# Optimization experiments

Hardware: AMD Instinct MI355X
Metric: run time of the kernel (lower is better)

## Reference

```python
import jax, jax.numpy as jnp
import numpy as np

N, P, C, M = 64, 8732, 91, 20          # batch, n_priors (SSD300), n_classes, padded objects/image
THRESHOLD = 0.5
NEG_POS_RATIO = 3
ALPHA = 1.0


def setup_inputs() -> dict:
    key = jax.random.key(0)
    k = jax.random.split(key, 7)
    predicted_locs = jax.random.normal(k[0], (N, P, 4), jnp.float32)
    predicted_scores = jax.random.normal(k[1], (N, P, C), jnp.float32)
    # ground-truth boxes in boundary (x1,y1,x2,y2) format, valid fractional coords
    xy = jax.random.uniform(k[2], (N, M, 2), minval=0.0, maxval=0.6)
    wh = jax.random.uniform(k[3], (N, M, 2), minval=0.05, maxval=0.4)
    boxes = jnp.concatenate([xy, xy + wh], axis=-1)
    labels = jax.random.randint(k[4], (N, M), 1, C).astype(jnp.int32)  # 0 = background
    # prior boxes in center-size (cx,cy,w,h) format
    cxy = jax.random.uniform(k[5], (P, 2), minval=0.05, maxval=0.95)
    pwh = jax.random.uniform(k[6], (P, 2), minval=0.05, maxval=0.3)
    priors_cxcy = jnp.concatenate([cxy, pwh], axis=-1)
    return dict(predicted_locs=predicted_locs, predicted_scores=predicted_scores,
                boxes=boxes, labels=labels, priors_cxcy=priors_cxcy)


def _iou(a, b):
    # a: (M,4) xyxy, b: (P,4) xyxy -> (M,P)
    lo = jnp.maximum(a[:, None, :2], b[None, :, :2])
    hi = jnp.minimum(a[:, None, 2:], b[None, :, 2:])
    inter = jnp.clip(hi - lo, 0.0).prod(-1)
    area_a = (a[:, 2:] - a[:, :2]).prod(-1)
    area_b = (b[:, 2:] - b[:, :2]).prod(-1)
    return inter / (area_a[:, None] + area_b[None, :] - inter)


def _xy_to_cxcy(xy):
    return jnp.concatenate([(xy[..., :2] + xy[..., 2:]) * 0.5, xy[..., 2:] - xy[..., :2]], -1)


def _cxcy_to_gcxgcy(cxcy, priors):
    g_cxcy = (cxcy[..., :2] - priors[..., :2]) / (priors[..., 2:] / 10.0)
    g_wh = jnp.log(cxcy[..., 2:] / priors[..., 2:]) * 5.0
    return jnp.concatenate([g_cxcy, g_wh], -1)


def _match_one(boxes_i, labels_i, priors_cxcy, priors_xy):
    overlap = _iou(boxes_i, priors_xy)                    # (M, P)
    ov_per_prior = overlap.max(0)                         # (P,)
    obj_per_prior = overlap.argmax(0)                     # (P,)
    prior_per_obj = overlap.argmax(1)                     # (M,)
    # force each object onto its best prior with overlap 1
    obj_per_prior = obj_per_prior.at[prior_per_obj].set(jnp.arange(M))
    ov_per_prior = ov_per_prior.at[prior_per_obj].set(1.0)
    label_per_prior = labels_i[obj_per_prior]             # (P,)
    label_per_prior = jnp.where(ov_per_prior < THRESHOLD, 0, label_per_prior)
    true_locs = _cxcy_to_gcxgcy(_xy_to_cxcy(boxes_i[obj_per_prior]), priors_cxcy)  # (P,4)
    return label_per_prior, true_locs


def reference(predicted_locs, predicted_scores, boxes, labels, priors_cxcy):
    priors_xy = jnp.concatenate([priors_cxcy[:, :2] - priors_cxcy[:, 2:] * 0.5,
                                 priors_cxcy[:, :2] + priors_cxcy[:, 2:] * 0.5], -1)
    true_classes, true_locs = jax.vmap(_match_one, in_axes=(0, 0, None, None))(
        boxes, labels, priors_cxcy, priors_xy)            # (N,P), (N,P,4)

    pos = true_classes != 0                               # (N, P)
    n_pos = pos.sum(1)                                    # (N,)
    n_pos_total = n_pos.sum().astype(jnp.float32)

    # localization: smooth L1 (beta=1), mean over positive elements
    d = predicted_locs - true_locs
    sl1 = jnp.where(jnp.abs(d) < 1.0, 0.5 * d * d, jnp.abs(d) - 0.5)   # (N,P,4)
    loc_loss = (sl1 * pos[..., None]).sum() / (n_pos_total * 4.0)

    # confidence: per-prior cross entropy
    logp = jax.nn.log_softmax(predicted_scores, axis=-1)  # (N,P,C)
    ce = -jnp.take_along_axis(logp, true_classes[..., None], axis=-1)[..., 0]  # (N,P)

    conf_loss_pos = (ce * pos).sum()
    # hard negative mining: sort negative losses desc, take 3*n_pos per image
    ce_neg = jnp.where(pos, 0.0, ce)
    ce_neg_sorted = jnp.sort(ce_neg, axis=1)[:, ::-1]     # (N,P) descending
    hard_neg = jnp.arange(P)[None, :] < (NEG_POS_RATIO * n_pos)[:, None]
    conf_loss_hard_neg = (ce_neg_sorted * hard_neg).sum()

    conf_loss = (conf_loss_pos + conf_loss_hard_neg) / n_pos_total
    return conf_loss + ALPHA * loc_loss
```

## Files before the change

### kernel.cpp

```cpp
#include <hip/hip_runtime.h>

#define NN 64
#define PP 8732
#define CC 91
#define MM 20
#define RATIO 3
#define BPI 8
#define CHUNK 1092
#define ROWS 128
#define BTHR 512
#define TILES2 ((NN * PP) / ROWS)

typedef unsigned long long u64;

__global__ __launch_bounds__(256) void match_a(
    const float4* __restrict__ boxes4,
    const float4* __restrict__ priors4,
    float* __restrict__ iou_out,
    unsigned char* __restrict__ obj8,
    u64* __restrict__ combined_part)
{
  __shared__ float bx0[MM], by0[MM], bx1[MM], by1[MM], ba[MM];
  __shared__ u64 wkey[4][MM];
  const int blk = blockIdx.x, tid = threadIdx.x;
  const int wave = tid >> 6, lane = tid & 63;
  const int n = blk >> 3, part = blk & 7;
  const int c0 = part * CHUNK;
  const int cend = (c0 + CHUNK < PP) ? c0 + CHUNK : PP;

  if (tid < MM) {
    float4 b = boxes4[n * MM + tid];
    bx0[tid] = b.x; by0[tid] = b.y; bx1[tid] = b.z; by1[tid] = b.w;
    ba[tid] = (b.z - b.x) * (b.w - b.y);
  }
  __syncthreads();

  float bi[MM], bd[MM]; int bpp[MM];
#pragma unroll
  for (int m = 0; m < MM; ++m) { bi[m] = 0.0f; bd[m] = 1.0f; bpp[m] = 0; }

#pragma unroll
  for (int i = 0; i < 5; ++i) {
    int p = c0 + tid + i * 256;
    if (p < cend) {
      float4 pr = priors4[p];
      float hw = pr.z * 0.5f, hh = pr.w * 0.5f;
      float px0 = pr.x - hw, py0 = pr.y - hh, px1 = pr.x + hw, py1 = pr.y + hh;
      float pa = (px1 - px0) * (py1 - py0);
      float pi = -1.0f, pd = 1.0f; int pm = 0;
#pragma unroll
      for (int m = 0; m < MM; ++m) {
        float iw = fminf(bx1[m], px1) - fmaxf(bx0[m], px0);
        float ih = fminf(by1[m], py1) - fmaxf(by0[m], py0);
        iw = fmaxf(iw, 0.0f); ih = fmaxf(ih, 0.0f);
        float inter = iw * ih;
        float den = (ba[m] + pa) - inter;
        bool c1 = inter * pd > pi * den;
        pi = c1 ? inter : pi; pd = c1 ? den : pd; pm = c1 ? m : pm;
        bool c2 = inter * bd[m] > bi[m] * den;
        bi[m] = c2 ? inter : bi[m]; bd[m] = c2 ? den : bd[m];
        bpp[m] = c2 ? p : bpp[m];
      }
      iou_out[(size_t)n * PP + p] = pi / pd;
      obj8[(size_t)n * PP + p] = (unsigned char)pm;
    }
  }

#pragma unroll
  for (int m = 0; m < MM; ++m) {
    float r = bi[m] / bd[m];
    u64 key = ((u64)__float_as_uint(r) << 32) | (unsigned)(~(unsigned)bpp[m]);
#pragma unroll
    for (int d = 1; d < 64; d <<= 1) {
      u64 o = __shfl_xor(key, d);
      key = (o > key) ? o : key;
    }
    if (lane == 0) wkey[wave][m] = key;
  }
  __syncthreads();
  if (tid < MM) {
    u64 best = wkey[0][tid];
    u64 o1 = wkey[1][tid], o2 = wkey[2][tid], o3 = wkey[3][tid];
    best = (o1 > best) ? o1 : best;
    best = (o2 > best) ? o2 : best;
    best = (o3 > best) ? o3 : best;
    combined_part[blk * MM + tid] = best;
  }
}

__global__ __launch_bounds__(BTHR) void ce_kernel(
    const float* __restrict__ scores,
    const float4* __restrict__ pred_locs4,
    const float4* __restrict__ priors4,
    const float4* __restrict__ boxes4,
    const int* __restrict__ labels,
    const float* __restrict__ iou,
    const unsigned char* __restrict__ obj8,
    const u64* __restrict__ combined_part,
    float* __restrict__ ce_neg,
    float4* __restrict__ partials)
{
  __shared__ unsigned key_lo[2][MM];
  __shared__ int lbl_s[2][MM];
  __shared__ float4 box_s[2][MM];
  __shared__ float4 w8[8];
  const int tid = threadIdx.x;
  const long base = (long)blockIdx.x * ROWS;
  const int n0 = (int)(base / PP);
  const int rem0 = (int)(base - (long)n0 * PP);
  const int r = tid >> 2, l = tid & 3;
  const long row = base + r;

  const float riou = iou[row];
  const int robj = obj8[row];

  if (tid < MM) {
    const u64* cp = combined_part + (size_t)n0 * BPI * MM;
    u64 best = cp[tid];
#pragma unroll
    for (int w = 1; w < BPI; ++w) {
      u64 o = cp[w * MM + tid];
      best = (o > best) ? o : best;
    }
    key_lo[0][tid] = (unsigned)best;
    lbl_s[0][tid]  = labels[n0 * MM + tid];
    box_s[0][tid]  = boxes4[n0 * MM + tid];
  } else if (tid >= 64 && tid < 64 + MM) {
    int j = tid - 64, nn = (n0 + 1 < NN) ? n0 + 1 : NN - 1;
    const u64* cp = combined_part + (size_t)nn * BPI * MM;
    u64 best = cp[j];
#pragma unroll
    for (int w = 1; w < BPI; ++w) {
      u64 o = cp[w * MM + j];
      best = (o > best) ? o : best;
    }
    key_lo[1][j] = (unsigned)best;
    lbl_s[1][j]  = labels[nn * MM + j];
    box_s[1][j]  = boxes4[nn * MM + j];
  }

  const float* rp = scores + (size_t)row * CC;
  float ss0 = 0.f, ss1 = 0.f, ss2 = 0.f, ss3 = 0.f;
#pragma unroll
  for (int j = 0; j < 23; ++j) {
    int c = l + 4 * j;
    if (c < CC) {
      float e = __expf(rp[c]);
      if ((j & 3) == 0) ss0 += e;
      else if ((j & 3) == 1) ss1 += e;
      else if ((j & 3) == 2) ss2 += e;
      else ss3 += e;
    }
  }
  float s = (ss0 + ss1) + (ss2 + ss3);
  s += __shfl_xor(s, 1);
  s += __shfl_xor(s, 2);

  __syncthreads();

  float cp_ = 0.0f, lp_ = 0.0f; int pos0 = 0, pos1 = 0;
  if (l == 0) {
    const int bn = (rem0 + r >= PP) ? 1 : 0;
    const int p = rem0 + r - bn * PP;
    int mm_ = -1;
    const unsigned want = ~(unsigned)p;
#pragma unroll
    for (int j = 0; j < MM; ++j) if (key_lo[bn][j] == want) mm_ = j;
    bool pos; int lab, sm;
    if (mm_ >= 0) { pos = true; sm = mm_; lab = lbl_s[bn][mm_]; }
    else {
      pos = !(riou < 0.5f);
      sm = robj; lab = pos ? lbl_s[bn][robj] : 0;
    }
    float ce = __logf(s) - rp[lab];
    if (pos) {
      cp_ = ce; ce_neg[row] = 0.0f;
      if (bn) pos1 = 1; else pos0 = 1;
      float4 bx = box_s[bn][sm], pr = priors4[p], pl = pred_locs4[row];
      float cx = (bx.x + bx.z) * 0.5f, cy = (bx.y + bx.w) * 0.5f;
      float w = bx.z - bx.x, h = bx.w - bx.y;
      float gx = (cx - pr.x) / (pr.z / 10.0f);
      float gy = (cy - pr.y) / (pr.w / 10.0f);
      float gz = __logf(w / pr.z) * 5.0f;
      float gw = __logf(h / pr.w) * 5.0f;
      float d, a;
      d = pl.x - gx; a = fabsf(d); lp_ += (a < 1.0f) ? 0.5f * d * d : a - 0.5f;
      d = pl.y - gy; a = fabsf(d); lp_ += (a < 1.0f) ? 0.5f * d * d : a - 0.5f;
      d = pl.z - gz; a = fabsf(d); lp_ += (a < 1.0f) ? 0.5f * d * d : a - 0.5f;
      d = pl.w - gw; a = fabsf(d); lp_ += (a < 1.0f) ? 0.5f * d * d : a - 0.5f;
    } else {
      ce_neg[row] = fmaxf(ce, 0.0f);
    }
  }

#pragma unroll
  for (int d = 1; d < 64; d <<= 1) {
    cp_ += __shfl_xor(cp_, d); lp_ += __shfl_xor(lp_, d);
    pos0 += __shfl_xor(pos0, d); pos1 += __shfl_xor(pos1, d);
  }
  if ((tid & 63) == 0)
    w8[tid >> 6] = make_float4(cp_, lp_, (float)pos0, (float)pos1);
  __syncthreads();
  if (tid == 0) {
    float sx = 0.f, sy = 0.f, sz = 0.f, sw = 0.f;
#pragma unroll
    for (int w = 0; w < 8; ++w) {
      sx += w8[w].x; sy += w8[w].y; sz += w8[w].z; sw += w8[w].w;
    }
    partials[blockIdx.x] = make_float4(sx, sy, sz, sw);
  }
}

__global__ __launch_bounds__(256) void hardneg_kernel(
    const float* __restrict__ ce_neg, const float4* __restrict__ partials,
    float* __restrict__ hard_sum)
{
  __shared__ int wred[2][4];
  __shared__ float wredf[4];
  __shared__ int wcnt[4];
  __shared__ float wk[4];
  const int n = blockIdx.x, tid = threadIdx.x;

  unsigned uv[35];
#pragma unroll
  for (int i = 0; i < 35; ++i) {
    int p = tid + i * 256;
    uv[i] = (p < PP) ? __float_as_uint(ce_neg[(size_t)n * PP + p]) : 0u;
  }

  {
    const int bstart = (n * PP) / ROWS;
    const int bend = (n * PP + PP - 1) / ROWS;
    float kc = 0.0f;
    for (int b = bstart + tid; b <= bend; b += 256) {
      float4 pb = partials[b];
      int nb0 = (b * ROWS) / PP;
      if (nb0 == n)     kc += pb.z;
      if (nb0 + 1 == n) kc += pb.w;
    }
#pragma unroll
    for (int d = 1; d < 64; d <<= 1) kc += __shfl_xor(kc, d);
    if ((tid & 63) == 0) wk[tid >> 6] = kc;
    __syncthreads();
  }
  const int k = RATIO * (int)(wk[0] + wk[1] + wk[2] + wk[3] + 0.5f);

  if (k <= 0) { if (tid == 0) hard_sum[n] = 0.0f; return; }

  if (k >= PP) {
    float s = 0.0f;
#pragma unroll
    for (int i = 0; i < 35; ++i) s += __uint_as_float(uv[i]);
#pragma unroll
    for (int d = 1; d < 64; d <<= 1) s += __shfl_xor(s, d);
    if ((tid & 63) == 0) wredf[tid >> 6] = s;
    __syncthreads();
    if (tid == 0) hard_sum[n] = wredf[0] + wredf[1] + wredf[2] + wredf[3];
    return;
  }

  unsigned lo = 0u, hi = 0x7f7fffffu;
  int it = 0;
  while (lo < hi) {
    unsigned mid = lo + ((hi - lo + 1u) >> 1);
    int c = 0;
#pragma unroll
    for (int i = 0; i < 35; ++i) c += (uv[i] >= mid);
#pragma unroll
    for (int d = 1; d < 64; d <<= 1) c += __shfl_xor(c, d);
    const int buf = it & 1;
    if ((tid & 63) == 0) wred[buf][tid >> 6] = c;
    __syncthreads();
    int total = wred[buf][0] + wred[buf][1] + wred[buf][2] + wred[buf][3];
    if (total >= k) lo = mid; else hi = mid - 1u;
    ++it;
  }
  const float x = __uint_as_float(lo);

  float s = 0.0f; int c = 0;
#pragma unroll
  for (int i = 0; i < 35; ++i) {
    unsigned b = uv[i];
    if (b > lo) { s += __uint_as_float(b); ++c; }
  }
#pragma unroll
  for (int d = 1; d < 64; d <<= 1) { s += __shfl_xor(s, d); c += __shfl_xor(c, d); }
  if ((tid & 63) == 0) { wredf[tid >> 6] = s; wcnt[tid >> 6] = c; }
  __syncthreads();
  if (tid == 0) {
    float st = wredf[0] + wredf[1] + wredf[2] + wredf[3];
    int   ct = wcnt[0] + wcnt[1] + wcnt[2] + wcnt[3];
    hard_sum[n] = st + (float)(k - ct) * x;
  }
}

__global__ __launch_bounds__(256) void final_kernel(
    const float4* __restrict__ partials, const float* __restrict__ hard_sum,
    float* __restrict__ out)
{
  __shared__ float4 w4[4];
  const int tid = threadIdx.x;
  float cp = 0.0f, lp = 0.0f, np = 0.0f;
  for (int i = tid; i < TILES2; i += 256) {
    float4 v = partials[i];
    cp += v.x; lp += v.y; np += v.z + v.w;
  }
  float hs = (tid < NN) ? hard_sum[tid] : 0.0f;
#pragma unroll
  for (int d = 1; d < 64; d <<= 1) {
    cp += __shfl_xor(cp, d); lp += __shfl_xor(lp, d);
    np += __shfl_xor(np, d); hs += __shfl_xor(hs, d);
  }
  if ((tid & 63) == 0) w4[tid >> 6] = make_float4(cp, lp, np, hs);
  __syncthreads();
  if (tid == 0) {
    float cpt = w4[0].x + w4[1].x + w4[2].x + w4[3].x;
    float lpt = w4[0].y + w4[1].y + w4[2].y + w4[3].y;
    float npt = w4[0].z + w4[1].z + w4[2].z + w4[3].z;
    float hst = w4[0].w + w4[1].w + w4[2].w + w4[3].w;
    out[0] = (cpt + hst) / npt + lpt / (npt * 4.0f);
  }
}

extern "C" void kernel_launch(void* const* d_in, const int* in_sizes, int n_in,
                              void* d_out, int out_size, void* d_ws, size_t ws_size,
                              hipStream_t stream) {
  const float*  pred_locs   = (const float*)d_in[0];
  const float*  pred_scores = (const float*)d_in[1];
  const float*  boxes       = (const float*)d_in[2];
  const int*    labels      = (const int*)d_in[3];
  const float*  priors      = (const float*)d_in[4];
  float* out = (float*)d_out;

  float* iou_ws = (float*)d_ws;
  float4* partials = (float4*)(iou_ws + (size_t)NN * PP);
  float*  ce_neg = (float*)(partials + TILES2);
  u64* combined_part = (u64*)(ce_neg + (size_t)NN * PP);
  float*  hard_sum = (float*)(combined_part + NN * BPI * MM);
  unsigned char* obj8 = (unsigned char*)(hard_sum + NN);

  match_a<<<NN * BPI, 256, 0, stream>>>((const float4*)boxes,
                                        (const float4*)priors,
                                        iou_ws, obj8, combined_part);
  ce_kernel<<<TILES2, BTHR, 0, stream>>>(pred_scores, (const float4*)pred_locs,
                                         (const float4*)priors,
                                         (const float4*)boxes, labels,
                                         iou_ws, obj8, combined_part,
                                         ce_neg, partials);
  hardneg_kernel<<<NN, 256, 0, stream>>>(ce_neg, partials, hard_sum);
  final_kernel<<<1, 256, 0, stream>>>(partials, hard_sum, out);
}
```

Measured before the change: 84.86 us.

## Pack match info into u16, fuse final reduction, use 4-way threshold search

The matching kernel now writes a packed 16-bit record (object index and thresholded label) in place of a float IoU plus a byte object index, which cuts the traffic between kernels. The final reduction kernel is folded into the hard-negative kernel through a last-block atomic counter, which removes one launch. The per-image threshold search now tests three pivots per iteration, so it needs about half as many block-wide barriers. The cost is more compare work per iteration, and the result now depends on a correct counter reset and on the threadfence ordering.

```diff
diff --git a/kernel.cpp b/kernel.cpp
--- a/kernel.cpp
+++ b/kernel.cpp
@@ -12,15 +12,18 @@
 #define TILES2 ((NN * PP) / ROWS)
 
 typedef unsigned long long u64;
+typedef unsigned short u16;
 
 __global__ __launch_bounds__(256) void match_a(
     const float4* __restrict__ boxes4,
     const float4* __restrict__ priors4,
-    float* __restrict__ iou_out,
-    unsigned char* __restrict__ obj8,
-    u64* __restrict__ combined_part)
+    const int* __restrict__ labels,
+    u16* __restrict__ minfo,
+    u64* __restrict__ combined_part,
+    int* __restrict__ counter)
 {
   __shared__ float bx0[MM], by0[MM], bx1[MM], by1[MM], ba[MM];
+  __shared__ int lb[MM];
   __shared__ u64 wkey[4][MM];
   const int blk = blockIdx.x, tid = threadIdx.x;
   const int wave = tid >> 6, lane = tid & 63;
@@ -28,10 +31,13 @@
   const int c0 = part * CHUNK;
   const int cend = (c0 + CHUNK < PP) ? c0 + CHUNK : PP;
 
+  if (blk == 0 && tid == 0) counter[0] = 0;
+
   if (tid < MM) {
     float4 b = boxes4[n * MM + tid];
     bx0[tid] = b.x; by0[tid] = b.y; bx1[tid] = b.z; by1[tid] = b.w;
     ba[tid] = (b.z - b.x) * (b.w - b.y);
+    lb[tid] = labels[n * MM + tid];
   }
   __syncthreads();
 
@@ -61,8 +67,9 @@
         bi[m] = c2 ? inter : bi[m]; bd[m] = c2 ? den : bd[m];
         bpp[m] = c2 ? p : bpp[m];
       }
-      iou_out[(size_t)n * PP + p] = pi / pd;
-      obj8[(size_t)n * PP + p] = (unsigned char)pm;
+      float q = pi / pd;
+      int lab8 = (q < 0.5f) ? 0 : lb[pm];
+      minfo[(size_t)n * PP + p] = (u16)((pm << 8) | lab8);
     }
   }
 
@@ -94,8 +101,7 @@
     const float4* __restrict__ priors4,
     const float4* __restrict__ boxes4,
     const int* __restrict__ labels,
-    const float* __restrict__ iou,
-    const unsigned char* __restrict__ obj8,
+    const u16* __restrict__ minfo,
     const u64* __restrict__ combined_part,
     float* __restrict__ ce_neg,
     float4* __restrict__ partials)
@@ -111,17 +117,13 @@
   const int r = tid >> 2, l = tid & 3;
   const long row = base + r;
 
-  const float riou = iou[row];
-  const int robj = obj8[row];
+  const int mi = minfo[row];
 
   if (tid < MM) {
     const u64* cp = combined_part + (size_t)n0 * BPI * MM;
     u64 best = cp[tid];
 #pragma unroll
-    for (int w = 1; w < BPI; ++w) {
-      u64 o = cp[w * MM + tid];
-      best = (o > best) ? o : best;
-    }
+    for (int w = 1; w < BPI; ++w) { u64 o = cp[w * MM + tid]; best = (o > best) ? o : best; }
     key_lo[0][tid] = (unsigned)best;
     lbl_s[0][tid]  = labels[n0 * MM + tid];
     box_s[0][tid]  = boxes4[n0 * MM + tid];
@@ -130,10 +132,7 @@
     const u64* cp = combined_part + (size_t)nn * BPI * MM;
     u64 best = cp[j];
 #pragma unroll
-    for (int w = 1; w < BPI; ++w) {
-      u64 o = cp[w * MM + j];
-      best = (o > best) ? o : best;
-    }
+    for (int w = 1; w < BPI; ++w) { u64 o = cp[w * MM + j]; best = (o > best) ? o : best; }
     key_lo[1][j] = (unsigned)best;
     lbl_s[1][j]  = labels[nn * MM + j];
     box_s[1][j]  = boxes4[nn * MM + j];
@@ -168,10 +167,7 @@
     for (int j = 0; j < MM; ++j) if (key_lo[bn][j] == want) mm_ = j;
     bool pos; int lab, sm;
     if (mm_ >= 0) { pos = true; sm = mm_; lab = lbl_s[bn][mm_]; }
-    else {
-      pos = !(riou < 0.5f);
-      sm = robj; lab = pos ? lbl_s[bn][robj] : 0;
-    }
+    else { lab = mi & 0xff; pos = (lab != 0); sm = mi >> 8; }
     float ce = __logf(s) - rp[lab];
     if (pos) {
       cp_ = ce; ce_neg[row] = 0.0f;
@@ -204,121 +200,135 @@
   if (tid == 0) {
     float sx = 0.f, sy = 0.f, sz = 0.f, sw = 0.f;
 #pragma unroll
-    for (int w = 0; w < 8; ++w) {
-      sx += w8[w].x; sy += w8[w].y; sz += w8[w].z; sw += w8[w].w;
-    }
+    for (int w = 0; w < 8; ++w) { sx += w8[w].x; sy += w8[w].y; sz += w8[w].z; sw += w8[w].w; }
     partials[blockIdx.x] = make_float4(sx, sy, sz, sw);
   }
 }
 
 __global__ __launch_bounds__(256) void hardneg_kernel(
     const float* __restrict__ ce_neg, const float4* __restrict__ partials,
-    float* __restrict__ hard_sum)
+    float4* __restrict__ per_img, int* __restrict__ counter,
+    float* __restrict__ out)
 {
-  __shared__ int wred[2][4];
+  __shared__ int4 cred[2][4];
   __shared__ float wredf[4];
   __shared__ int wcnt[4];
-  __shared__ float wk[4];
+  __shared__ float4 wacc[4];
+  __shared__ int last_s;
   const int n = blockIdx.x, tid = threadIdx.x;
 
   unsigned uv[35];
 #pragma unroll
   for (int i = 0; i < 35; ++i) {
-    int p = tid + i * 256;
+    int p = tid + (i << 8);
     uv[i] = (p < PP) ? __float_as_uint(ce_neg[(size_t)n * PP + p]) : 0u;
   }
 
+  float kc = 0.0f, cpo = 0.0f, lpo = 0.0f;
   {
     const int bstart = (n * PP) / ROWS;
-    const int bend = (n * PP + PP - 1) / ROWS;
-    float kc = 0.0f;
+    const int bend = ((n + 1) * PP - 1) / ROWS;
+    const int ost = (n * PP + ROWS - 1) / ROWS;
+    const int oen = ((n + 1) * PP + ROWS - 1) / ROWS;
     for (int b = bstart + tid; b <= bend; b += 256) {
       float4 pb = partials[b];
       int nb0 = (b * ROWS) / PP;
       if (nb0 == n)     kc += pb.z;
       if (nb0 + 1 == n) kc += pb.w;
-    }
-#pragma unroll
-    for (int d = 1; d < 64; d <<= 1) kc += __shfl_xor(kc, d);
-    if ((tid & 63) == 0) wk[tid >> 6] = kc;
-    __syncthreads();
-  }
-  const int k = RATIO * (int)(wk[0] + wk[1] + wk[2] + wk[3] + 0.5f);
-
-  if (k <= 0) { if (tid == 0) hard_sum[n] = 0.0f; return; }
-
+      if (b >= ost && b < oen) { cpo += pb.x; lpo += pb.y; }
+    }
+#pragma unroll
+    for (int d = 1; d < 64; d <<= 1) {
+      kc += __shfl_xor(kc, d); cpo += __shfl_xor(cpo, d); lpo += __shfl_xor(lpo, d);
+    }
+    if ((tid & 63) == 0) wacc[tid >> 6] = make_float4(kc, cpo, lpo, 0.f);
+    __syncthreads();
+    kc = wacc[0].x + wacc[1].x + wacc[2].x + wacc[3].x;
+    cpo = wacc[0].y + wacc[1].y + wacc[2].y + wacc[3].y;
+    lpo = wacc[0].z + wacc[1].z + wacc[2].z + wacc[3].z;
+  }
+  const float npn = kc;
+  const int k = RATIO * (int)(kc + 0.5f);
+
+  float hs = 0.0f;
   if (k >= PP) {
     float s = 0.0f;
 #pragma unroll
     for (int i = 0; i < 35; ++i) s += __uint_as_float(uv[i]);
 #pragma unroll
     for (int d = 1; d < 64; d <<= 1) s += __shfl_xor(s, d);
+    __syncthreads();
     if ((tid & 63) == 0) wredf[tid >> 6] = s;
     __syncthreads();
-    if (tid == 0) hard_sum[n] = wredf[0] + wredf[1] + wredf[2] + wredf[3];
-    return;
-  }
-
-  unsigned lo = 0u, hi = 0x7f7fffffu;
-  int it = 0;
-  while (lo < hi) {
-    unsigned mid = lo + ((hi - lo + 1u) >> 1);
-    int c = 0;
-#pragma unroll
-    for (int i = 0; i < 35; ++i) c += (uv[i] >= mid);
-#pragma unroll
-    for (int d = 1; d < 64; d <<= 1) c += __shfl_xor(c, d);
-    const int buf = it & 1;
-    if ((tid & 63) == 0) wred[buf][tid >> 6] = c;
-    __syncthreads();
-    int total = wred[buf][0] + wred[buf][1] + wred[buf][2] + wred[buf][3];
-    if (total >= k) lo = mid; else hi = mid - 1u;
-    ++it;
-  }
-  const float x = __uint_as_float(lo);
-
-  float s = 0.0f; int c = 0;
-#pragma unroll
-  for (int i = 0; i < 35; ++i) {
-    unsigned b = uv[i];
-    if (b > lo) { s += __uint_as_float(b); ++c; }
-  }
-#pragma unroll
-  for (int d = 1; d < 64; d <<= 1) { s += __shfl_xor(s, d); c += __shfl_xor(c, d); }
-  if ((tid & 63) == 0) { wredf[tid >> 6] = s; wcnt[tid >> 6] = c; }
-  __syncthreads();
+    hs = wredf[0] + wredf[1] + wredf[2] + wredf[3];
+  } else if (k > 0) {
+    unsigned lo = 0u, hi = 0x7f7fffffu;
+    int it = 0;
+    while (lo < hi) {
+      unsigned span = hi - lo;
+      unsigned q4 = span >> 2;
+      unsigned m1, m2, m3;
+      if (q4 == 0) { m1 = m2 = m3 = lo + ((span + 1) >> 1); }
+      else { m1 = lo + q4; m2 = lo + 2 * q4; m3 = lo + 3 * q4; }
+      int a1 = 0, a2 = 0, a3 = 0;
+#pragma unroll
+      for (int i = 0; i < 35; ++i) {
+        unsigned v = uv[i];
+        a1 += (v >= m1); a2 += (v >= m2); a3 += (v >= m3);
+      }
+#pragma unroll
+      for (int d = 1; d < 64; d <<= 1) {
+        a1 += __shfl_xor(a1, d); a2 += __shfl_xor(a2, d); a3 += __shfl_xor(a3, d);
+      }
+      const int buf = it & 1;
+      if ((tid & 63) == 0) cred[buf][tid >> 6] = make_int4(a1, a2, a3, 0);
+      __syncthreads();
+      int c1 = 0, c2 = 0, c3 = 0;
+#pragma unroll
+      for (int w = 0; w < 4; ++w) {
+        int4 cc = cred[buf][w];
+        c1 += cc.x; c2 += cc.y; c3 += cc.z;
+      }
+      if (c3 >= k) lo = m3;
+      else if (c2 >= k) { lo = m2; hi = m3 - 1; }
+      else if (c1 >= k) { lo = m1; hi = m2 - 1; }
+      else hi = m1 - 1;
+      ++it;
+    }
+    const float x = __uint_as_float(lo);
+    float s = 0.0f; int c = 0;
+#pragma unroll
+    for (int i = 0; i < 35; ++i) {
+      unsigned v = uv[i];
+      if (v > lo) { s += __uint_as_float(v); ++c; }
+    }
+#pragma unroll
+    for (int d = 1; d < 64; d <<= 1) { s += __shfl_xor(s, d); c += __shfl_xor(c, d); }
+    __syncthreads();
+    if ((tid & 63) == 0) { wredf[tid >> 6] = s; wcnt[tid >> 6] = c; }
+    __syncthreads();
+    hs = (wredf[0] + wredf[1] + wredf[2] + wredf[3]) +
+         (float)(k - (wcnt[0] + wcnt[1] + wcnt[2] + wcnt[3])) * x;
+  }
+
   if (tid == 0) {
-    float st = wredf[0] + wredf[1] + wredf[2] + wredf[3];
-    int   ct = wcnt[0] + wcnt[1] + wcnt[2] + wcnt[3];
-    hard_sum[n] = st + (float)(k - ct) * x;
-  }
-}
-
-__global__ __launch_bounds__(256) void final_kernel(
-    const float4* __restrict__ partials, const float* __restrict__ hard_sum,
-    float* __restrict__ out)
-{
-  __shared__ float4 w4[4];
-  const int tid = threadIdx.x;
-  float cp = 0.0f, lp = 0.0f, np = 0.0f;
-  for (int i = tid; i < TILES2; i += 256) {
-    float4 v = partials[i];
-    cp += v.x; lp += v.y; np += v.z + v.w;
-  }
-  float hs = (tid < NN) ? hard_sum[tid] : 0.0f;
-#pragma unroll
-  for (int d = 1; d < 64; d <<= 1) {
-    cp += __shfl_xor(cp, d); lp += __shfl_xor(lp, d);
-    np += __shfl_xor(np, d); hs += __shfl_xor(hs, d);
-  }
-  if ((tid & 63) == 0) w4[tid >> 6] = make_float4(cp, lp, np, hs);
-  __syncthreads();
-  if (tid == 0) {
-    float cpt = w4[0].x + w4[1].x + w4[2].x + w4[3].x;
-    float lpt = w4[0].y + w4[1].y + w4[2].y + w4[3].y;
-    float npt = w4[0].z + w4[1].z + w4[2].z + w4[3].z;
-    float hst = w4[0].w + w4[1].w + w4[2].w + w4[3].w;
-    out[0] = (cpt + hst) / npt + lpt / (npt * 4.0f);
+    per_img[n] = make_float4(cpo, lpo, npn, hs);
+    __threadfence();
+    last_s = atomicAdd(counter, 1);
+  }
+  __syncthreads();
+  if (last_s == NN - 1) {
+    __threadfence();
+    if (tid < 64) {
+      float4 v = per_img[tid];
+      float a = v.x, b = v.y, c = v.z, d = v.w;
+#pragma unroll
+      for (int dd = 1; dd < 64; dd <<= 1) {
+        a += __shfl_xor(a, dd); b += __shfl_xor(b, dd);
+        c += __shfl_xor(c, dd); d += __shfl_xor(d, dd);
+      }
+      if (tid == 0) out[0] = (a + d) / c + b / (c * 4.0f);
+    }
   }
 }
 
@@ -332,21 +342,20 @@
   const float*  priors      = (const float*)d_in[4];
   float* out = (float*)d_out;
 
-  float* iou_ws = (float*)d_ws;
-  float4* partials = (float4*)(iou_ws + (size_t)NN * PP);
+  u16* minfo = (u16*)d_ws;
+  float4* partials = (float4*)(minfo + (size_t)NN * PP);
   float*  ce_neg = (float*)(partials + TILES2);
   u64* combined_part = (u64*)(ce_neg + (size_t)NN * PP);
-  float*  hard_sum = (float*)(combined_part + NN * BPI * MM);
-  unsigned char* obj8 = (unsigned char*)(hard_sum + NN);
+  float4* per_img = (float4*)(combined_part + NN * BPI * MM);
+  int* counter = (int*)(per_img + NN);
 
   match_a<<<NN * BPI, 256, 0, stream>>>((const float4*)boxes,
-                                        (const float4*)priors,
-                                        iou_ws, obj8, combined_part);
+                                        (const float4*)priors, labels,
+                                        minfo, combined_part, counter);
   ce_kernel<<<TILES2, BTHR, 0, stream>>>(pred_scores, (const float4*)pred_locs,
                                          (const float4*)priors,
                                          (const float4*)boxes, labels,
-                                         iou_ws, obj8, combined_part,
+                                         minfo, combined_part,
                                          ce_neg, partials);
-  hardneg_kernel<<<NN, 256, 0, stream>>>(ce_neg, partials, hard_sum);
-  final_kernel<<<1, 256, 0, stream>>>(partials, hard_sum, out);
+  hardneg_kernel<<<NN, 256, 0, stream>>>(ce_neg, partials, per_img, counter, out);
 }
```

New measurement: 83.75 us. No clear change (-1.3%).
